# Performance work log

Hardware: AMD Instinct MI355X
Metric: run time of the kernel (lower is better)

Reference implementation:

```python
import jax, jax.numpy as jnp
import numpy as np

N, M, B, L, C, H = 4096, 16384, 8, 96, 512, 8
Dh = C // H


def setup_inputs() -> dict:
    key0 = jax.random.key(0)
    ks = jax.random.split(key0, 8)
    query = jax.random.normal(ks[0], (N, C), dtype=jnp.float32)
    key_t = jax.random.normal(ks[1], (M, C), dtype=jnp.float32)
    value = jax.random.normal(ks[2], (M, C), dtype=jnp.float32)
    keys_per_batch = M // B  # 2048 local key indices per scene
    idx = jax.random.randint(ks[3], (N, L), 0, keys_per_batch)
    pad = jax.random.uniform(ks[4], (N, L)) < 0.1
    pad = pad.at[:, 0].set(False)
    index_pair = jnp.where(pad, -1, idx).astype(jnp.int64)
    query_batch_cnt = jnp.full((B,), N // B, dtype=jnp.int32)
    key_batch_cnt = jnp.full((B,), M // B, dtype=jnp.int32)
    index_pair_batch = jnp.repeat(jnp.arange(B, dtype=jnp.int64), N // B)
    in_proj_weight = jax.random.normal(ks[5], (3 * C, C), dtype=jnp.float32) * (1.0 / np.sqrt(C))
    in_proj_bias = jnp.zeros((3 * C,), dtype=jnp.float32)
    out_proj_weight = jax.random.normal(ks[6], (C, C), dtype=jnp.float32) * (1.0 / np.sqrt(C))
    out_proj_bias = jnp.zeros((C,), dtype=jnp.float32)
    return {
        "query": query, "key": key_t, "value": value,
        "index_pair": index_pair, "query_batch_cnt": query_batch_cnt,
        "key_batch_cnt": key_batch_cnt, "index_pair_batch": index_pair_batch,
        "in_proj_weight": in_proj_weight, "in_proj_bias": in_proj_bias,
        "out_proj_weight": out_proj_weight, "out_proj_bias": out_proj_bias,
    }


def reference(query, key, value, index_pair, query_batch_cnt, key_batch_cnt,
              index_pair_batch, in_proj_weight, in_proj_bias,
              out_proj_weight, out_proj_bias):
    n, c = query.shape
    l = index_pair.shape[1]
    scaling = float(Dh) ** -0.5
    # QKV projections (F.linear: x @ W.T + b)
    q = query @ in_proj_weight[:c].T + in_proj_bias[:c]
    k = key @ in_proj_weight[c:2 * c].T + in_proj_bias[c:2 * c]
    v = value @ in_proj_weight[2 * c:].T + in_proj_bias[2 * c:]
    q = (q * scaling).reshape(n, H, Dh)
    k = k.reshape(-1, H, Dh)
    v = v.reshape(-1, H, Dh)
    mask = index_pair < 0  # (N, L)
    # convert local per-batch key index to global index via exclusive cumsum of key counts
    offs = jnp.concatenate([jnp.zeros((1,), key_batch_cnt.dtype), jnp.cumsum(key_batch_cnt)[:-1]])
    gidx = jnp.where(mask, 0, index_pair + offs[index_pair_batch][:, None])  # (N, L)
    k_g = k[gidx]  # (N, L, H, Dh)
    attn = jnp.einsum('nhd,nlhd->nlh', q, k_g)
    attn = jnp.where(mask[:, :, None], -jnp.inf, attn)
    attn = jax.nn.softmax(attn, axis=1)  # softmax over neighbor dim L
    v_g = v[gidx]  # (N, L, H, Dh)
    out = jnp.einsum('nlh,nlhd->nhd', attn, v_g).reshape(n, c)
    out = out @ out_proj_weight.T + out_proj_bias
    return out, attn.sum(axis=-1) / H
```

## Files before the change

kernel.cpp:

```cpp
#include <hip/hip_runtime.h>
#include <hip/hip_fp16.h>
#include <cstdint>
#include <cstddef>

#define N_Q 4096
#define M_K 16384
#define LNB 96
#define CH  512
#define NH  8

typedef _Float16 half8  __attribute__((ext_vector_type(8)));
typedef _Float16 h2     __attribute__((ext_vector_type(2)));
typedef float    floatx4 __attribute__((ext_vector_type(4)));
typedef float    floatx2 __attribute__((ext_vector_type(2)));

union H8 { half8 v; h2 p[4]; };

__device__ __forceinline__ h2 cvt2(float a, float b) {
    return __builtin_bit_cast(h2, __builtin_amdgcn_cvt_pkrtz(a, b));
}

__device__ __forceinline__ void async16(const void* g, void* l) {
    __builtin_amdgcn_global_load_lds(
        (const __attribute__((address_space(1))) void*)g,
        (__attribute__((address_space(3))) void*)l, 16, 0, 0);
}

template<int CTRL>
__device__ __forceinline__ float dpp_addf(float x) {
    int xi = __builtin_bit_cast(int, x);
    int yi = __builtin_amdgcn_update_dpp(xi, xi, CTRL, 0xF, 0xF, false);
    return x + __builtin_bit_cast(float, yi);
}
__device__ __forceinline__ float octet_sum(float x) {
    x = dpp_addf<0x141>(x);
    x = dpp_addf<0x4E>(x);
    x = dpp_addf<0xB1>(x);
    return x;
}

__global__ void cvt_weights(const float* __restrict__ wIn, const float* __restrict__ wOut,
                            _Float16* __restrict__ dst) {
    const size_t i = (size_t)blockIdx.x * blockDim.x + threadIdx.x;
    const float4 v = (i < 196608) ? ((const float4*)wIn)[i]
                                  : ((const float4*)wOut)[i - 196608];
    h2 a = cvt2(v.x, v.y);
    h2 b = cvt2(v.z, v.w);
    *(h2*)&dst[i * 4]     = a;
    *(h2*)&dst[i * 4 + 2] = b;
}

template<int OUTF16, int TM, int AFP32>
__device__ __forceinline__ void gemm_body(
    const void* __restrict__ Ap, const _Float16* __restrict__ Bw,
    const float* __restrict__ bias, void* __restrict__ outp, float oscale,
    int bm, int bn)
{
    constexpr int MI = TM / 32;
    __shared__ alignas(16) _Float16 As[TM * 32];
    __shared__ alignas(16) _Float16 Bs[128 * 32];

    const int t    = threadIdx.x;
    const int lane = t & 63;
    const int wave = t >> 6;
    const int wm   = wave >> 1, wn = wave & 1;

    floatx4 acc[MI][4] = {};

    const int rowL = t >> 2;
    const int kcol = (t & 3) * 8;
    const _Float16* gB = Bw + (size_t)(bn * 128 + rowL) * CH + kcol;
    _Float16* lB = &Bs[rowL * 32 + kcol];

    const _Float16* gA16 = nullptr; _Float16* lA16 = nullptr;
    const float* gA32 = nullptr; _Float16* lA32 = nullptr;
    if constexpr (AFP32) {
        const int arow = (TM == 128) ? (t >> 1) : (t >> 2);
        const int ac0  = (TM == 128) ? ((t & 1) * 16) : ((t & 3) * 8);
        gA32 = (const float*)Ap + (size_t)(bm * TM + arow) * CH + ac0;
        lA32 = &As[arow * 32 + ac0];
    } else {
        gA16 = (const _Float16*)Ap + (size_t)(bm * TM + rowL) * CH + kcol;
        lA16 = &As[rowL * 32 + kcol];
    }

    const int r0 = lane & 15;
    const int ko = (lane >> 4) * 8;

    for (int kt = 0; kt < CH / 32; ++kt) {
        if constexpr (AFP32) {
            const float* ga = gA32 + kt * 32;
            if constexpr (TM == 128) {
                float4 x0 = ((const float4*)ga)[0], x1 = ((const float4*)ga)[1];
                float4 x2 = ((const float4*)ga)[2], x3 = ((const float4*)ga)[3];
                H8 o0, o1;
                o0.p[0] = cvt2(x0.x, x0.y);
                o0.p[1] = cvt2(x0.z, x0.w);
                o0.p[2] = cvt2(x1.x, x1.y);
                o0.p[3] = cvt2(x1.z, x1.w);
                o1.p[0] = cvt2(x2.x, x2.y);
                o1.p[1] = cvt2(x2.z, x2.w);
                o1.p[2] = cvt2(x3.x, x3.y);
                o1.p[3] = cvt2(x3.z, x3.w);
                *(half8*)lA32       = o0.v;
                *(half8*)(lA32 + 8) = o1.v;
            } else {
                float4 x0 = ((const float4*)ga)[0], x1 = ((const float4*)ga)[1];
                H8 o0;
                o0.p[0] = cvt2(x0.x, x0.y);
                o0.p[1] = cvt2(x0.z, x0.w);
                o0.p[2] = cvt2(x1.x, x1.y);
                o0.p[3] = cvt2(x1.z, x1.w);
                *(half8*)lA32 = o0.v;
            }
        } else {
            const _Float16* a0 = gA16 + kt * 32;
            async16(a0, lA16);
            if constexpr (TM == 128) async16(a0 + 64 * CH, lA16 + 64 * 32);
        }
        const _Float16* b0 = gB + kt * 32;
        async16(b0,           lB);
        async16(b0 + 64 * CH, lB + 64 * 32);
        __syncthreads();

        half8 af[MI], bf[4];
        #pragma unroll
        for (int mi = 0; mi < MI; ++mi)
            af[mi] = *(const half8*)&As[(wm * (TM / 2) + mi * 16 + r0) * 32 + ko];
        #pragma unroll
        for (int ni = 0; ni < 4; ++ni)
            bf[ni] = *(const half8*)&Bs[(wn * 64 + ni * 16 + r0) * 32 + ko];
        #pragma unroll
        for (int mi = 0; mi < MI; ++mi)
            #pragma unroll
            for (int ni = 0; ni < 4; ++ni)
                acc[mi][ni] = __builtin_amdgcn_mfma_f32_16x16x32_f16(
                    af[mi], bf[ni], acc[mi][ni], 0, 0, 0);
        __syncthreads();
    }

    #pragma unroll
    for (int mi = 0; mi < MI; ++mi) {
        #pragma unroll
        for (int ni = 0; ni < 4; ++ni) {
            const int col = bn * 128 + wn * 64 + ni * 16 + (lane & 15);
            const float bv = bias[col];
            #pragma unroll
            for (int r = 0; r < 4; ++r) {
                const int row = bm * TM + wm * (TM / 2) + mi * 16 + (lane >> 4) * 4 + r;
                const float v = (acc[mi][ni][r] + bv) * oscale;
                if (OUTF16) ((_Float16*)outp)[(size_t)row * CH + col] = (_Float16)v;
                else        ((float*)outp)[(size_t)row * CH + col]    = v;
            }
        }
    }
}

template<int OUTF16, int TM, int AFP32>
__global__ __launch_bounds__(256) void gemm_k(
    const void* __restrict__ A, const _Float16* __restrict__ Bw,
    const float* __restrict__ bias, void* __restrict__ outp, float oscale)
{
    gemm_body<OUTF16, TM, AFP32>(A, Bw, bias, outp, oscale, blockIdx.x, blockIdx.y);
}

__global__ __launch_bounds__(256) void gemm_kv(
    const float* __restrict__ keyp, const float* __restrict__ valp,
    const _Float16* __restrict__ w16, const float* __restrict__ bIn,
    _Float16* __restrict__ k16, _Float16* __restrict__ v16)
{
    const int z = blockIdx.z;
    gemm_body<1, 128, 1>(z ? (const void*)valp : (const void*)keyp,
                         w16 + (size_t)(z ? 1024 : 512) * 512,
                         bIn + (z ? 1024 : 512),
                         z ? (void*)v16 : (void*)k16, 1.0f,
                         blockIdx.x, blockIdx.y);
}

__global__ __launch_bounds__(256) void attn_kernel(
    const _Float16* __restrict__ q16, const _Float16* __restrict__ k16,
    const _Float16* __restrict__ v16, const int* __restrict__ ipair,
    const int* __restrict__ ibatch, const int* __restrict__ kcnt,
    _Float16* __restrict__ op16, float* __restrict__ aout)
{
    __shared__ uint32_t vmask[LNB];
    __shared__ float    pls[LNB * 9];
    __shared__ __half2  pph[LNB * 9];
    __shared__ float    part[4][CH];

    const int t = threadIdx.x;
    const int n = ((blockIdx.x & 7) << 9) | (blockIdx.x >> 3);

    if (t < LNB) {
        const int idx = ipair[(size_t)n * LNB + t];
        const int b   = ibatch[n];
        int off = 0;
        for (int i = 0; i < b; ++i) off += kcnt[i];
        const uint32_t vo = (uint32_t)((idx < 0 ? 0 : (idx + off)) * (CH * 2));
        vmask[t] = vo | (idx < 0 ? 0x80000000u : 0u);
    }
    __syncthreads();

    const int lane = t & 63, wv = t >> 6;
    const int h    = lane >> 3;
    const int l0   = wv * 24;

    {
        const half8 qv = *(const half8*)(q16 + (size_t)n * CH + lane * 8);
        H8 qu; qu.v = qv;
        const char* kbase = (const char*)k16 + lane * 16;
        const int4* vb = (const int4*)&vmask[l0];
        for (int g = 0; g < 3; ++g) {
            const int4 w0 = vb[2 * g], w1 = vb[2 * g + 1];
            uint32_t vm8[8] = {(uint32_t)w0.x, (uint32_t)w0.y, (uint32_t)w0.z, (uint32_t)w0.w,
                               (uint32_t)w1.x, (uint32_t)w1.y, (uint32_t)w1.z, (uint32_t)w1.w};
            #pragma unroll
            for (int j = 0; j < 8; ++j) {
                const uint32_t vms = __builtin_amdgcn_readfirstlane(vm8[j]);
                H8 ku; ku.v = *(const half8*)(kbase + (vms & 0x7fffffffu));
                float acc = 0.f;
                #pragma unroll
                for (int u = 0; u < 4; ++u)
                    acc = __builtin_amdgcn_fdot2(qu.p[u], ku.p[u], acc, false);
                acc = octet_sum(acc);
                if ((lane & 7) == 0)
                    pls[(l0 + g * 8 + j) * 9 + h] = (vms & 0x80000000u) ? -1e30f : acc;
            }
        }
    }
    __syncthreads();

    {
        const int hh = t >> 5, j = t & 31;
        const float v0 = pls[j * 9 + hh];
        const float v1 = pls[(j + 32) * 9 + hh];
        const float v2 = pls[(j + 64) * 9 + hh];
        float m = fmaxf(v0, fmaxf(v1, v2));
        #pragma unroll
        for (int s = 16; s >= 1; s >>= 1) m = fmaxf(m, __shfl_xor(m, s, 32));
        const float e0 = __expf(v0 - m), e1 = __expf(v1 - m), e2 = __expf(v2 - m);
        float ssum = e0 + e1 + e2;
        #pragma unroll
        for (int s = 16; s >= 1; s >>= 1) ssum += __shfl_xor(ssum, s, 32);
        const float rinv = 1.0f / ssum;
        const float p0 = e0 * rinv, p1 = e1 * rinv, p2 = e2 * rinv;
        pls[j * 9 + hh]        = p0;
        pls[(j + 32) * 9 + hh] = p1;
        pls[(j + 64) * 9 + hh] = p2;
        pph[j * 9 + hh]        = __half2half2(__float2half_rn(p0));
        pph[(j + 32) * 9 + hh] = __half2half2(__float2half_rn(p1));
        pph[(j + 64) * 9 + hh] = __half2half2(__float2half_rn(p2));
    }
    __syncthreads();

    if (t < LNB) {
        float s = 0.f;
        #pragma unroll
        for (int u = 0; u < NH; ++u) s += pls[t * 9 + u];
        aout[(size_t)n * LNB + t] = s * (1.0f / NH);
    }

    {
        float accf[8] = {};
        const char* vbase = (const char*)v16 + lane * 16;
        const int4* vb = (const int4*)&vmask[l0];
        const __half2 hz = __half2half2(__float2half_rn(0.f));
        for (int g = 0; g < 3; ++g) {
            const int4 w0 = vb[2 * g], w1 = vb[2 * g + 1];
            uint32_t vm8[8] = {(uint32_t)w0.x, (uint32_t)w0.y, (uint32_t)w0.z, (uint32_t)w0.w,
                               (uint32_t)w1.x, (uint32_t)w1.y, (uint32_t)w1.z, (uint32_t)w1.w};
            __half2 a0 = hz, a1 = hz, a2 = hz, a3 = hz;
            #pragma unroll
            for (int j = 0; j < 8; ++j) {
                const uint32_t vms = __builtin_amdgcn_readfirstlane(vm8[j]);
                const half8 vv = *(const half8*)(vbase + (vms & 0x7fffffffu));
                union { half8 v; __half2 q[4]; } vu; vu.v = vv;
                const __half2 pp = pph[(l0 + g * 8 + j) * 9 + h];
                a0 = __hfma2(pp, vu.q[0], a0);
                a1 = __hfma2(pp, vu.q[1], a1);
                a2 = __hfma2(pp, vu.q[2], a2);
                a3 = __hfma2(pp, vu.q[3], a3);
            }
            float2 f;
            f = __half22float2(a0); accf[0] += f.x; accf[1] += f.y;
            f = __half22float2(a1); accf[2] += f.x; accf[3] += f.y;
            f = __half22float2(a2); accf[4] += f.x; accf[5] += f.y;
            f = __half22float2(a3); accf[6] += f.x; accf[7] += f.y;
        }
        floatx4 lo, hi;
        #pragma unroll
        for (int u = 0; u < 4; ++u) { lo[u] = accf[u]; hi[u] = accf[u + 4]; }
        *(floatx4*)&part[wv][lane * 8]     = lo;
        *(floatx4*)&part[wv][lane * 8 + 4] = hi;
    }
    __syncthreads();

    {
        const int c = t * 2;
        floatx2 s = *(const floatx2*)&part[0][c];
        #pragma unroll
        for (int w = 1; w < 4; ++w) {
            floatx2 pw = *(const floatx2*)&part[w][c];
            s[0] += pw[0]; s[1] += pw[1];
        }
        h2 o; o[0] = (_Float16)s[0]; o[1] = (_Float16)s[1];
        *(h2*)&op16[(size_t)n * CH + c] = o;
    }
}

extern "C" void kernel_launch(void* const* d_in, const int* in_sizes, int n_in,
                              void* d_out, int out_size, void* d_ws, size_t ws_size,
                              hipStream_t stream)
{
    const float* query = (const float*)d_in[0];
    const float* key   = (const float*)d_in[1];
    const float* value = (const float*)d_in[2];
    const int*   ipair = (const int*)d_in[3];
    const int*   kcnt  = (const int*)d_in[5];
    const int*   ibat  = (const int*)d_in[6];
    const float* wIn   = (const float*)d_in[7];
    const float* bIn   = (const float*)d_in[8];
    const float* wOut  = (const float*)d_in[9];
    const float* bOut  = (const float*)d_in[10];

    float* out  = (float*)d_out;
    float* aout = out + (size_t)N_Q * CH;

    char* ws = (char*)d_ws;
    _Float16* w16  = (_Float16*)(ws);
    _Float16* wo16 = (_Float16*)(ws + 1572864);
    _Float16* q16  = (_Float16*)(ws + 2097152);
    _Float16* k16  = (_Float16*)(ws + 6291456);
    _Float16* v16  = (_Float16*)(ws + 23068672);
    _Float16* op16 = (_Float16*)(ws + 39845888);

    cvt_weights<<<1024, 256, 0, stream>>>(wIn, wOut, w16);

    gemm_k<1, 64, 1><<<dim3(64, 4), 256, 0, stream>>>(query, w16, bIn, q16, 0.125f);
    gemm_kv<<<dim3(128, 4, 2), 256, 0, stream>>>(key, value, w16, bIn, k16, v16);

    attn_kernel<<<4096, 256, 0, stream>>>(q16, k16, v16, ipair, ibat, kcnt, op16, aout);

    gemm_k<0, 64, 0><<<dim3(64, 4), 256, 0, stream>>>(op16, wo16, bOut, d_out, 1.0f);
}
```

Baseline: 113.8 us.

## Rewrite K/V projection GEMM with register prefetch, BK=64 and swizzled LDS

The K/V projection GEMM stops using the generic body and gets a dedicated kernel. It uses a K-tile of 64 and XOR-swizzled shared-memory layouts to avoid bank conflicts. Global loads for the next tile go into registers while MFMAs run on the current tile, so fp32 load latency overlaps compute and there are half as many barriers. The generic body loses its TM=128 paths, and the extra prefetch registers may lower occupancy.

Measured after the change: 143.4 us. +26.0%, slower.

```diff
diff --git a/kernel.cpp b/kernel.cpp
--- a/kernel.cpp
+++ b/kernel.cpp
@@ -75,10 +75,8 @@
     const _Float16* gA16 = nullptr; _Float16* lA16 = nullptr;
     const float* gA32 = nullptr; _Float16* lA32 = nullptr;
     if constexpr (AFP32) {
-        const int arow = (TM == 128) ? (t >> 1) : (t >> 2);
-        const int ac0  = (TM == 128) ? ((t & 1) * 16) : ((t & 3) * 8);
-        gA32 = (const float*)Ap + (size_t)(bm * TM + arow) * CH + ac0;
-        lA32 = &As[arow * 32 + ac0];
+        gA32 = (const float*)Ap + (size_t)(bm * TM + rowL) * CH + kcol;
+        lA32 = &As[rowL * 32 + kcol];
     } else {
         gA16 = (const _Float16*)Ap + (size_t)(bm * TM + rowL) * CH + kcol;
         lA16 = &As[rowL * 32 + kcol];
@@ -90,33 +88,16 @@
     for (int kt = 0; kt < CH / 32; ++kt) {
         if constexpr (AFP32) {
             const float* ga = gA32 + kt * 32;
-            if constexpr (TM == 128) {
-                float4 x0 = ((const float4*)ga)[0], x1 = ((const float4*)ga)[1];
-                float4 x2 = ((const float4*)ga)[2], x3 = ((const float4*)ga)[3];
-                H8 o0, o1;
-                o0.p[0] = cvt2(x0.x, x0.y);
-                o0.p[1] = cvt2(x0.z, x0.w);
-                o0.p[2] = cvt2(x1.x, x1.y);
-                o0.p[3] = cvt2(x1.z, x1.w);
-                o1.p[0] = cvt2(x2.x, x2.y);
-                o1.p[1] = cvt2(x2.z, x2.w);
-                o1.p[2] = cvt2(x3.x, x3.y);
-                o1.p[3] = cvt2(x3.z, x3.w);
-                *(half8*)lA32       = o0.v;
-                *(half8*)(lA32 + 8) = o1.v;
-            } else {
-                float4 x0 = ((const float4*)ga)[0], x1 = ((const float4*)ga)[1];
-                H8 o0;
-                o0.p[0] = cvt2(x0.x, x0.y);
-                o0.p[1] = cvt2(x0.z, x0.w);
-                o0.p[2] = cvt2(x1.x, x1.y);
-                o0.p[3] = cvt2(x1.z, x1.w);
-                *(half8*)lA32 = o0.v;
-            }
+            float4 x0 = ((const float4*)ga)[0], x1 = ((const float4*)ga)[1];
+            H8 o0;
+            o0.p[0] = cvt2(x0.x, x0.y);
+            o0.p[1] = cvt2(x0.z, x0.w);
+            o0.p[2] = cvt2(x1.x, x1.y);
+            o0.p[3] = cvt2(x1.z, x1.w);
+            *(half8*)lA32 = o0.v;
         } else {
             const _Float16* a0 = gA16 + kt * 32;
             async16(a0, lA16);
-            if constexpr (TM == 128) async16(a0 + 64 * CH, lA16 + 64 * 32);
         }
         const _Float16* b0 = gB + kt * 32;
         async16(b0,           lB);
@@ -170,11 +151,99 @@
     _Float16* __restrict__ k16, _Float16* __restrict__ v16)
 {
     const int z = blockIdx.z;
-    gemm_body<1, 128, 1>(z ? (const void*)valp : (const void*)keyp,
-                         w16 + (size_t)(z ? 1024 : 512) * 512,
-                         bIn + (z ? 1024 : 512),
-                         z ? (void*)v16 : (void*)k16, 1.0f,
-                         blockIdx.x, blockIdx.y);
+    const float*    Ap   = z ? valp : keyp;
+    const _Float16* Bw   = w16 + (size_t)(z ? 1024 : 512) * 512;
+    const float*    bias = bIn + (z ? 1024 : 512);
+    _Float16*       outp = z ? v16 : k16;
+    const int bm = blockIdx.x, bn = blockIdx.y;
+
+    __shared__ alignas(16) _Float16 As[128 * 64];
+    __shared__ alignas(16) _Float16 Bs[128 * 64];
+
+    const int t    = threadIdx.x;
+    const int lane = t & 63;
+    const int wave = t >> 6;
+    const int wm   = wave >> 1, wn = wave & 1;
+
+    const int r2   = t >> 1;
+    const int hf   = t & 1;
+    const int swzr = r2 & 7;
+    const float*    gA = Ap + (size_t)(bm * 128 + r2) * CH + hf * 32;
+    const _Float16* gB = Bw + (size_t)(bn * 128 + r2) * CH + hf * 32;
+    _Float16* wA = &As[r2 * 64];
+    _Float16* wB = &Bs[r2 * 64];
+
+    floatx4 acc[4][4] = {};
+    float4 ab[8]; int4 bb[4];
+
+    #pragma unroll
+    for (int i = 0; i < 8; ++i) ab[i] = ((const float4*)gA)[i];
+    #pragma unroll
+    for (int i = 0; i < 4; ++i) bb[i] = ((const int4*)gB)[i];
+
+    const int r0 = lane & 15, hi = lane >> 4;
+    const int rsw = r0 & 7;
+
+    for (int kt = 0; kt < 8; ++kt) {
+        #pragma unroll
+        for (int i2 = 0; i2 < 4; ++i2) {
+            H8 o;
+            o.p[0] = cvt2(ab[2*i2].x,   ab[2*i2].y);
+            o.p[1] = cvt2(ab[2*i2].z,   ab[2*i2].w);
+            o.p[2] = cvt2(ab[2*i2+1].x, ab[2*i2+1].y);
+            o.p[3] = cvt2(ab[2*i2+1].z, ab[2*i2+1].w);
+            const int g = hf * 4 + i2;
+            *(half8*)&wA[(g ^ swzr) * 8] = o.v;
+        }
+        #pragma unroll
+        for (int i = 0; i < 4; ++i) {
+            const int g = hf * 4 + i;
+            *(int4*)&wB[(g ^ swzr) * 8] = bb[i];
+        }
+        __syncthreads();
+
+        if (kt < 7) {
+            const float*    ga = gA + (kt + 1) * 64;
+            const _Float16* gb = gB + (kt + 1) * 64;
+            #pragma unroll
+            for (int i = 0; i < 8; ++i) ab[i] = ((const float4*)ga)[i];
+            #pragma unroll
+            for (int i = 0; i < 4; ++i) bb[i] = ((const int4*)gb)[i];
+        }
+
+        #pragma unroll
+        for (int kh = 0; kh < 2; ++kh) {
+            half8 af[4], bf[4];
+            const int gg = kh * 4 + hi;
+            #pragma unroll
+            for (int mi = 0; mi < 4; ++mi)
+                af[mi] = *(const half8*)&As[(wm * 64 + mi * 16 + r0) * 64 + ((gg ^ rsw) * 8)];
+            #pragma unroll
+            for (int ni = 0; ni < 4; ++ni)
+                bf[ni] = *(const half8*)&Bs[(wn * 64 + ni * 16 + r0) * 64 + ((gg ^ rsw) * 8)];
+            #pragma unroll
+            for (int mi = 0; mi < 4; ++mi)
+                #pragma unroll
+                for (int ni = 0; ni < 4; ++ni)
+                    acc[mi][ni] = __builtin_amdgcn_mfma_f32_16x16x32_f16(
+                        af[mi], bf[ni], acc[mi][ni], 0, 0, 0);
+        }
+        __syncthreads();
+    }
+
+    #pragma unroll
+    for (int mi = 0; mi < 4; ++mi) {
+        #pragma unroll
+        for (int ni = 0; ni < 4; ++ni) {
+            const int col = bn * 128 + wn * 64 + ni * 16 + (lane & 15);
+            const float bv = bias[col];
+            #pragma unroll
+            for (int r = 0; r < 4; ++r) {
+                const int row = bm * 128 + wm * 64 + mi * 16 + (lane >> 4) * 4 + r;
+                outp[(size_t)row * CH + col] = (_Float16)(acc[mi][ni][r] + bv);
+            }
+        }
+    }
 }
 
 __global__ __launch_bounds__(256) void attn_kernel(
@@ -337,6 +406,7 @@
     cvt_weights<<<1024, 256, 0, stream>>>(wIn, wOut, w16);
 
     gemm_k<1, 64, 1><<<dim3(64, 4), 256, 0, stream>>>(query, w16, bIn, q16, 0.125f);
+
     gemm_kv<<<dim3(128, 4, 2), 256, 0, stream>>>(key, value, w16, bIn, k16, v16);
 
     attn_kernel<<<4096, 256, 0, stream>>>(q16, k16, v16, ipair, ibat, kcnt, op16, aout);
```

## Restructure projection GEMMs into full-width 128x512 tiles with swizzled async LDS loads

Applied to the files above, without the earlier changes.

Replaces the 128-column GEMM tiles with 512-thread blocks that each compute a 128-row by full 512-column output tile. fp32 activations are now loaded asynchronously into LDS with an XOR swizzle and converted to fp16 at fragment-read time. The Q, K and V projections are merged into a single launch. The aim is to read each A row once instead of four times and to cut launch overhead. The trade-off is far fewer blocks (288 for QKV, only 32 for the output projection), which risks underfilling the 256 CUs, plus higher register and LDS use per block.

After: 125.8 us. 10.5% more time.

```diff
diff --git a/kernel.cpp b/kernel.cpp
--- a/kernel.cpp
+++ b/kernel.cpp
@@ -50,131 +50,150 @@
     *(h2*)&dst[i * 4 + 2] = b;
 }
 
-template<int OUTF16, int TM, int AFP32>
-__device__ __forceinline__ void gemm_body(
-    const void* __restrict__ Ap, const _Float16* __restrict__ Bw,
-    const float* __restrict__ bias, void* __restrict__ outp, float oscale,
-    int bm, int bn)
-{
-    constexpr int MI = TM / 32;
-    __shared__ alignas(16) _Float16 As[TM * 32];
-    __shared__ alignas(16) _Float16 Bs[128 * 32];
+template<int AFP32, int OUTF16>
+__device__ __forceinline__ void wide_body(
+    const void* __restrict__ Asrc, const _Float16* __restrict__ W,
+    const float* __restrict__ bias, void* __restrict__ dst,
+    float oscale, int bm)
+{
+    __shared__ alignas(16) char As[16384];
+    __shared__ alignas(16) char Bs[32768];
+
+    const char* Ab = (const char*)Asrc;
+    const char* Bb = (const char*)W;
 
     const int t    = threadIdx.x;
     const int lane = t & 63;
-    const int wave = t >> 6;
-    const int wm   = wave >> 1, wn = wave & 1;
-
-    floatx4 acc[MI][4] = {};
-
-    const int rowL = t >> 2;
-    const int kcol = (t & 3) * 8;
-    const _Float16* gB = Bw + (size_t)(bn * 128 + rowL) * CH + kcol;
-    _Float16* lB = &Bs[rowL * 32 + kcol];
-
-    const _Float16* gA16 = nullptr; _Float16* lA16 = nullptr;
-    const float* gA32 = nullptr; _Float16* lA32 = nullptr;
+    const int wv   = t >> 6;
+    const int wm   = wv >> 2;
+    const int wn   = wv & 3;
+    const int r0   = lane & 15;
+    const int hi   = lane >> 4;
+
+    floatx4 acc[4][8] = {};
+
+    uint32_t aoff[2]; uint32_t alds[2];
     if constexpr (AFP32) {
-        const int arow = (TM == 128) ? (t >> 1) : (t >> 2);
-        const int ac0  = (TM == 128) ? ((t & 1) * 16) : ((t & 3) * 8);
-        gA32 = (const float*)Ap + (size_t)(bm * TM + arow) * CH + ac0;
-        lA32 = &As[arow * 32 + ac0];
+        #pragma unroll
+        for (int q = 0; q < 2; ++q) {
+            const int G   = q * 512 + t;
+            const int row = G >> 3;
+            const int g   = (G & 7) ^ (row & 7);
+            aoff[q] = (uint32_t)((bm * 128 + row) * 2048 + g * 16);
+            alds[q] = (uint32_t)G * 16;
+        }
     } else {
-        gA16 = (const _Float16*)Ap + (size_t)(bm * TM + rowL) * CH + kcol;
-        lA16 = &As[rowL * 32 + kcol];
-    }
-
-    const int r0 = lane & 15;
-    const int ko = (lane >> 4) * 8;
-
-    for (int kt = 0; kt < CH / 32; ++kt) {
+        const int G     = t;
+        const int super = G >> 3;
+        const int sgg   = (G & 7) ^ (super & 7);
+        const int row   = super * 2 + (sgg >> 2);
+        const int g     = sgg & 3;
+        aoff[0] = (uint32_t)((bm * 128 + row) * 1024 + g * 16);
+        alds[0] = (uint32_t)G * 16;
+        aoff[1] = 0; alds[1] = 0;
+    }
+    uint32_t boff[4]; uint32_t blds[4];
+    #pragma unroll
+    for (int q = 0; q < 4; ++q) {
+        const int G     = q * 512 + t;
+        const int super = G >> 3;
+        const int sgg   = (G & 7) ^ (super & 7);
+        const int row   = super * 2 + (sgg >> 2);
+        const int g     = sgg & 3;
+        boff[q] = (uint32_t)(row * 1024 + g * 16);
+        blds[q] = (uint32_t)G * 16;
+    }
+
+    for (int kt = 0; kt < 16; ++kt) {
         if constexpr (AFP32) {
-            const float* ga = gA32 + kt * 32;
-            if constexpr (TM == 128) {
-                float4 x0 = ((const float4*)ga)[0], x1 = ((const float4*)ga)[1];
-                float4 x2 = ((const float4*)ga)[2], x3 = ((const float4*)ga)[3];
-                H8 o0, o1;
-                o0.p[0] = cvt2(x0.x, x0.y);
-                o0.p[1] = cvt2(x0.z, x0.w);
-                o0.p[2] = cvt2(x1.x, x1.y);
-                o0.p[3] = cvt2(x1.z, x1.w);
-                o1.p[0] = cvt2(x2.x, x2.y);
-                o1.p[1] = cvt2(x2.z, x2.w);
-                o1.p[2] = cvt2(x3.x, x3.y);
-                o1.p[3] = cvt2(x3.z, x3.w);
-                *(half8*)lA32       = o0.v;
-                *(half8*)(lA32 + 8) = o1.v;
+            async16(Ab + aoff[0] + kt * 128, As + alds[0]);
+            async16(Ab + aoff[1] + kt * 128, As + alds[1]);
+        } else {
+            async16(Ab + aoff[0] + kt * 64, As + alds[0]);
+        }
+        #pragma unroll
+        for (int q = 0; q < 4; ++q)
+            async16(Bb + boff[q] + kt * 64, Bs + blds[q]);
+        __syncthreads();
+
+        half8 af[4], bf[8];
+        #pragma unroll
+        for (int mi = 0; mi < 4; ++mi) {
+            const int row = wm * 64 + mi * 16 + r0;
+            if constexpr (AFP32) {
+                const int swz = row & 7;
+                const float4 x0 = *(const float4*)(As + row * 128 + (((hi * 2)     ^ swz) * 16));
+                const float4 x1 = *(const float4*)(As + row * 128 + (((hi * 2 + 1) ^ swz) * 16));
+                H8 o;
+                o.p[0] = cvt2(x0.x, x0.y);
+                o.p[1] = cvt2(x0.z, x0.w);
+                o.p[2] = cvt2(x1.x, x1.y);
+                o.p[3] = cvt2(x1.z, x1.w);
+                af[mi] = o.v;
             } else {
-                float4 x0 = ((const float4*)ga)[0], x1 = ((const float4*)ga)[1];
-                H8 o0;
-                o0.p[0] = cvt2(x0.x, x0.y);
-                o0.p[1] = cvt2(x0.z, x0.w);
-                o0.p[2] = cvt2(x1.x, x1.y);
-                o0.p[3] = cvt2(x1.z, x1.w);
-                *(half8*)lA32 = o0.v;
+                const int super = row >> 1;
+                const int vv    = ((row & 1) * 4 + hi) ^ (super & 7);
+                af[mi] = *(const half8*)(As + super * 128 + vv * 16);
             }
-        } else {
-            const _Float16* a0 = gA16 + kt * 32;
-            async16(a0, lA16);
-            if constexpr (TM == 128) async16(a0 + 64 * CH, lA16 + 64 * 32);
-        }
-        const _Float16* b0 = gB + kt * 32;
-        async16(b0,           lB);
-        async16(b0 + 64 * CH, lB + 64 * 32);
-        __syncthreads();
-
-        half8 af[MI], bf[4];
-        #pragma unroll
-        for (int mi = 0; mi < MI; ++mi)
-            af[mi] = *(const half8*)&As[(wm * (TM / 2) + mi * 16 + r0) * 32 + ko];
-        #pragma unroll
-        for (int ni = 0; ni < 4; ++ni)
-            bf[ni] = *(const half8*)&Bs[(wn * 64 + ni * 16 + r0) * 32 + ko];
-        #pragma unroll
-        for (int mi = 0; mi < MI; ++mi)
+        }
+        #pragma unroll
+        for (int ni = 0; ni < 8; ++ni) {
+            const int row   = wn * 128 + ni * 16 + r0;
+            const int super = row >> 1;
+            const int vv    = ((row & 1) * 4 + hi) ^ (super & 7);
+            bf[ni] = *(const half8*)(Bs + super * 128 + vv * 16);
+        }
+        #pragma unroll
+        for (int mi = 0; mi < 4; ++mi)
             #pragma unroll
-            for (int ni = 0; ni < 4; ++ni)
+            for (int ni = 0; ni < 8; ++ni)
                 acc[mi][ni] = __builtin_amdgcn_mfma_f32_16x16x32_f16(
                     af[mi], bf[ni], acc[mi][ni], 0, 0, 0);
         __syncthreads();
     }
 
     #pragma unroll
-    for (int mi = 0; mi < MI; ++mi) {
-        #pragma unroll
-        for (int ni = 0; ni < 4; ++ni) {
-            const int col = bn * 128 + wn * 64 + ni * 16 + (lane & 15);
+    for (int mi = 0; mi < 4; ++mi) {
+        #pragma unroll
+        for (int ni = 0; ni < 8; ++ni) {
+            const int col = wn * 128 + ni * 16 + r0;
             const float bv = bias[col];
             #pragma unroll
             for (int r = 0; r < 4; ++r) {
-                const int row = bm * TM + wm * (TM / 2) + mi * 16 + (lane >> 4) * 4 + r;
+                const int row = bm * 128 + wm * 64 + mi * 16 + hi * 4 + r;
                 const float v = (acc[mi][ni][r] + bv) * oscale;
-                if (OUTF16) ((_Float16*)outp)[(size_t)row * CH + col] = (_Float16)v;
-                else        ((float*)outp)[(size_t)row * CH + col]    = v;
+                if (OUTF16) ((_Float16*)dst)[(size_t)row * CH + col] = (_Float16)v;
+                else        ((float*)dst)[(size_t)row * CH + col]    = v;
             }
         }
     }
 }
 
-template<int OUTF16, int TM, int AFP32>
-__global__ __launch_bounds__(256) void gemm_k(
-    const void* __restrict__ A, const _Float16* __restrict__ Bw,
-    const float* __restrict__ bias, void* __restrict__ outp, float oscale)
-{
-    gemm_body<OUTF16, TM, AFP32>(A, Bw, bias, outp, oscale, blockIdx.x, blockIdx.y);
-}
-
-__global__ __launch_bounds__(256) void gemm_kv(
-    const float* __restrict__ keyp, const float* __restrict__ valp,
-    const _Float16* __restrict__ w16, const float* __restrict__ bIn,
+__global__ __launch_bounds__(512) void proj_qkv(
+    const float* __restrict__ query, const float* __restrict__ keyp,
+    const float* __restrict__ valp, const _Float16* __restrict__ w16,
+    const float* __restrict__ bIn, _Float16* __restrict__ q16,
     _Float16* __restrict__ k16, _Float16* __restrict__ v16)
 {
-    const int z = blockIdx.z;
-    gemm_body<1, 128, 1>(z ? (const void*)valp : (const void*)keyp,
-                         w16 + (size_t)(z ? 1024 : 512) * 512,
-                         bIn + (z ? 1024 : 512),
-                         z ? (void*)v16 : (void*)k16, 1.0f,
-                         blockIdx.x, blockIdx.y);
+    const int bid = blockIdx.x;
+    if (bid < 32) {
+        wide_body<1, 1>(query, w16, bIn, q16, 0.125f, bid);
+    } else {
+        const int i  = bid - 32;
+        const int z  = i >> 7;
+        const int bm = i & 127;
+        wide_body<1, 1>(z ? (const void*)valp : (const void*)keyp,
+                        w16 + (size_t)(z ? 1024 : 512) * 512,
+                        bIn + (z ? 1024 : 512),
+                        z ? v16 : k16, 1.0f, bm);
+    }
+}
+
+__global__ __launch_bounds__(512) void proj_out(
+    const _Float16* __restrict__ op16, const _Float16* __restrict__ wo16,
+    const float* __restrict__ bOut, float* __restrict__ outp)
+{
+    wide_body<0, 0>(op16, wo16, bOut, outp, 1.0f, blockIdx.x);
 }
 
 __global__ __launch_bounds__(256) void attn_kernel(
@@ -336,10 +355,9 @@
 
     cvt_weights<<<1024, 256, 0, stream>>>(wIn, wOut, w16);
 
-    gemm_k<1, 64, 1><<<dim3(64, 4), 256, 0, stream>>>(query, w16, bIn, q16, 0.125f);
-    gemm_kv<<<dim3(128, 4, 2), 256, 0, stream>>>(key, value, w16, bIn, k16, v16);
+    proj_qkv<<<288, 512, 0, stream>>>(query, key, value, w16, bIn, q16, k16, v16);
 
     attn_kernel<<<4096, 256, 0, stream>>>(q16, k16, v16, ipair, ibat, kcnt, op16, aout);
 
-    gemm_k<0, 64, 0><<<dim3(64, 4), 256, 0, stream>>>(op16, wo16, bOut, d_out, 1.0f);
-}
+    proj_out<<<32, 512, 0, stream>>>(op16, wo16, bOut, (float*)d_out);
+}
```
